# Kernel tuning notes

Measured on AMD Instinct MI355X. Metric: run time of the kernel, lower is better.

## Reference

```python
import jax, jax.numpy as jnp
import numpy as np

D_MODEL = 1024
NUM_HEADS = 16
D_K = D_MODEL // NUM_HEADS
ROPE_THETA = 10000.0


def setup_inputs() -> dict:
    key = jax.random.key(0)
    kx, kq, kk, kv, ko = jax.random.split(key, 5)
    B, S = 4, 2048
    std = (2.0 / (D_MODEL + D_MODEL)) ** 0.5
    def w(k):
        return jax.random.truncated_normal(k, -3.0, 3.0, (D_MODEL, D_MODEL), jnp.float32) * std
    return {
        "x": jax.random.normal(kx, (B, S, D_MODEL), jnp.float32),
        "Wq": w(kq), "Wk": w(kk), "Wv": w(kv), "Wo": w(ko),
    }


def _apply_rope(t):
    # t: [B, H, S, d_k]
    S, dk = t.shape[-2], t.shape[-1]
    inv_freq = 1.0 / (ROPE_THETA ** (jnp.arange(0, dk, 2) / dk))  # [dk/2]
    angles = jnp.outer(jnp.arange(S), inv_freq)                    # [S, dk/2]
    cos = jnp.repeat(jnp.cos(angles), 2, axis=-1).astype(t.dtype)  # [S, dk]
    sin = jnp.repeat(jnp.sin(angles), 2, axis=-1).astype(t.dtype)
    t_even = t[..., 0::2]
    t_odd = t[..., 1::2]
    t_rot = jnp.stack([-t_odd, t_even], axis=-1).reshape(t.shape)
    return t * cos + t_rot * sin


def reference(x, Wq, Wk, Wv, Wo):
    B, S, D = x.shape
    H, dk = NUM_HEADS, D_K
    q = jnp.einsum("bsi,io->bso", x, Wq).reshape(B, S, H, dk).swapaxes(1, 2)
    k = jnp.einsum("bsi,io->bso", x, Wk).reshape(B, S, H, dk).swapaxes(1, 2)
    v = jnp.einsum("bsi,io->bso", x, Wv).reshape(B, S, H, dk).swapaxes(1, 2)
    q = _apply_rope(q)
    k = _apply_rope(k)
    scores = jnp.einsum("bhqd,bhkd->bhqk", q, k) / (dk ** 0.5)  # [B,H,S,S]
    causal = jnp.tril(jnp.ones((S, S), dtype=bool))
    scores = jnp.where(causal, scores, -jnp.inf)
    attn = jax.nn.softmax(scores, axis=-1)
    out = jnp.einsum("bhqk,bhkd->bhqd", attn, v)  # [B,H,S,dk]
    out = out.swapaxes(1, 2).reshape(B, S, D)
    return jnp.einsum("bsi,io->bso", out, Wo)
```

## Files before the change

### kernel.cpp

```cpp
#include <hip/hip_runtime.h>
#include <hip/hip_bf16.h>

#define SEQ   2048
#define NB    4
#define NH    16
#define DK    64
#define DM    1024
#define MROWS (NB * SEQ)
#define WEL   (DM * DM)

typedef __bf16 bf16_t;
typedef __bf16 bf16x8 __attribute__((ext_vector_type(8)));
typedef __bf16 bf16x4 __attribute__((ext_vector_type(4)));
typedef float  f32x4  __attribute__((ext_vector_type(4)));

#define MFMA16(a, b, c) __builtin_amdgcn_mfma_f32_16x16x32_bf16((a), (b), (c), 0, 0, 0)

__device__ __forceinline__ void gl2lds16(const bf16_t* g, bf16_t* l) {
    __builtin_amdgcn_global_load_lds(
        (const __attribute__((address_space(1))) unsigned int*)g,
        (__attribute__((address_space(3))) unsigned int*)l, 16, 0, 0);
}

#define BAR()   __builtin_amdgcn_s_barrier()
#define SCB()   __builtin_amdgcn_sched_barrier(0)
#define LGK0()  asm volatile("s_waitcnt lgkmcnt(0)")
#define LGK8()  asm volatile("s_waitcnt lgkmcnt(8)")
#define VMC(N)  asm volatile("s_waitcnt vmcnt(" #N ")")

__global__ __launch_bounds__(256) void prep_kernel(
    const float* __restrict__ x,
    const float* __restrict__ Wq, const float* __restrict__ Wk,
    const float* __restrict__ Wv, const float* __restrict__ Wo,
    bf16_t* __restrict__ xb, bf16_t* __restrict__ Wqkvt,
    bf16_t* __restrict__ Wot, float2* __restrict__ rope)
{
    __shared__ float T[32][33];
    const int bid = blockIdx.x;
    const int tid = threadIdx.x;

    if (bid < 8192) {
        const int i = (bid * 256 + tid) * 4;
        const float4 v = *(const float4*)(x + i);
        bf16x4 o;
        o[0] = (bf16_t)v.x; o[1] = (bf16_t)v.y;
        o[2] = (bf16_t)v.z; o[3] = (bf16_t)v.w;
        *(bf16x4*)(xb + i) = o;
    } else if (bid < 12288) {
        const int wb = bid - 8192;
        const int w  = wb >> 10;
        const int b10 = wb & 1023;
        const float* W = (w == 0) ? Wq : (w == 1) ? Wk : (w == 2) ? Wv : Wo;
        bf16_t* Wt = (w == 3) ? Wot : Wqkvt + (size_t)w * WEL;
        const int tk0 = (b10 >> 5) << 5;
        const int tn0 = (b10 & 31) << 5;
        const int r = tid >> 5, c = tid & 31;
#pragma unroll
        for (int i = 0; i < 4; ++i)
            T[r + i * 8][c] = W[(size_t)(tk0 + r + i * 8) * DM + tn0 + c];
        __syncthreads();
#pragma unroll
        for (int i = 0; i < 4; ++i)
            Wt[(size_t)(tn0 + r + i * 8) * DM + tk0 + c] = (bf16_t)T[c][r + i * 8];
    } else {
        const int idx = (bid - 12288) * 256 + tid;
        const int s = idx >> 5, i = idx & 31;
        const float freq = powf(10000.0f, -(float)i / 32.0f);
        const float a = (float)s * freq;
        rope[idx] = make_float2(cosf(a), sinf(a));
    }
}

template<bool TR>
__device__ __forceinline__ void kloop(
    const bf16_t* __restrict__ Xp, const bf16_t* __restrict__ Wp,
    bf16_t* L, int tid, f32x4 (&acc)[8][4])
{
    const int lane = tid & 63;
    const int wave = tid >> 6;
    const int wm   = wave >> 2;
    const int wn   = wave & 3;
    const int lrow = lane & 15;
    const int lcol = (lane >> 4) << 3;

    bf16_t* const AR = L;
    bf16_t* const BR = L + 32768;

    const bf16_t* pA0 = Xp + (size_t)(wave * 16 + lrow) * DM + lcol;
    const bf16_t* pA1 = pA0 + (size_t)128 * DM;
    const bf16_t* pB0 = Wp + (size_t)(wave * 16 + lrow) * DM + lcol;
    const bf16_t* pB1 = pB0 + (size_t)128 * DM;

    bf16_t* const adst = AR + wave * 1024;
    bf16_t* const bdst = BR + wave * 1024;

    const bf16_t* const Ard = AR + wm * 8192;
    const bf16_t* const Brd = BR + wn * 4096;

    bf16x8 a[2][2], bc[4][2];

#define RD_A(BUF, Q)                                                          \
    a[0][0] = *(const bf16x8*)(Ard + (BUF) + (2*(Q)+0)*1024 + lane*8);        \
    a[0][1] = *(const bf16x8*)(Ard + (BUF) + (2*(Q)+0)*1024 + 512 + lane*8);  \
    a[1][0] = *(const bf16x8*)(Ard + (BUF) + (2*(Q)+1)*1024 + lane*8);        \
    a[1][1] = *(const bf16x8*)(Ard + (BUF) + (2*(Q)+1)*1024 + 512 + lane*8);

#define RD_B(BUF, NF)                                                         \
    bc[NF][0] = *(const bf16x8*)(Brd + (BUF) + (NF)*1024 + lane*8);           \
    bc[NF][1] = *(const bf16x8*)(Brd + (BUF) + (NF)*1024 + 512 + lane*8);

#define ST_A(BUF, H, C)                                                       \
    gl2lds16(((H) ? pA1 : pA0) + (C),      adst + (BUF) + (H)*8192);          \
    gl2lds16(((H) ? pA1 : pA0) + (C) + 32, adst + (BUF) + (H)*8192 + 512);

#define ST_B(BUF, H, C)                                                       \
    gl2lds16(((H) ? pB1 : pB0) + (C),      bdst + (BUF) + (H)*8192);          \
    gl2lds16(((H) ? pB1 : pB0) + (C) + 32, bdst + (BUF) + (H)*8192 + 512);

#define QMMA(Q)                                                               \
    __builtin_amdgcn_s_setprio(1);                                            \
    _Pragma("unroll")                                                         \
    for (int nf = 0; nf < 4; ++nf) {                                          \
        if (TR) {                                                             \
            acc[2*(Q)][nf]   = MFMA16(bc[nf][0], a[0][0], acc[2*(Q)][nf]);    \
            acc[2*(Q)][nf]   = MFMA16(bc[nf][1], a[0][1], acc[2*(Q)][nf]);    \
            acc[2*(Q)+1][nf] = MFMA16(bc[nf][0], a[1][0], acc[2*(Q)+1][nf]);  \
            acc[2*(Q)+1][nf] = MFMA16(bc[nf][1], a[1][1], acc[2*(Q)+1][nf]);  \
        } else {                                                              \
            acc[2*(Q)][nf]   = MFMA16(a[0][0], bc[nf][0], acc[2*(Q)][nf]);    \
            acc[2*(Q)][nf]   = MFMA16(a[0][1], bc[nf][1], acc[2*(Q)][nf]);    \
            acc[2*(Q)+1][nf] = MFMA16(a[1][0], bc[nf][0], acc[2*(Q)+1][nf]);  \
            acc[2*(Q)+1][nf] = MFMA16(a[1][1], bc[nf][1], acc[2*(Q)+1][nf]);  \
        }                                                                     \
    }                                                                         \
    __builtin_amdgcn_s_setprio(0);

    ST_B(0, 0, 0)      ST_B(0, 1, 0)
    ST_A(0, 0, 0)      ST_A(0, 1, 0)
    ST_B(16384, 0, 64) ST_B(16384, 1, 64)
    VMC(4);
    BAR();

    for (int it = 0; it < 8; ++it) {
        const bool lst = (it == 7);

        RD_A(0, 0) RD_B(0, 0) RD_B(0, 1) RD_B(0, 2) RD_B(0, 3)
        ST_A(16384, 0, 64) ST_A(16384, 1, 64)
        LGK8();
        BAR(); LGK0(); SCB();
        QMMA(0)
        BAR();

        RD_A(0, 1)
        if (!lst) { ST_B(0, 0, 128) }
        BAR(); LGK0(); SCB();
        QMMA(1)
        BAR();

        RD_A(0, 2)
        if (!lst) { ST_B(0, 1, 128) }
        BAR(); LGK0(); SCB();
        QMMA(2)
        BAR();

        RD_A(0, 3)
        BAR(); LGK0(); SCB();
        QMMA(3)
        if (lst) { VMC(0); } else { VMC(4); }
        BAR();

        RD_A(16384, 0) RD_B(16384, 0) RD_B(16384, 1) RD_B(16384, 2) RD_B(16384, 3)
        if (!lst) { ST_A(0, 0, 128) }
        LGK8();
        BAR(); LGK0(); SCB();
        QMMA(0)
        BAR();

        RD_A(16384, 1)
        if (!lst) { ST_A(0, 1, 128) }
        BAR(); LGK0(); SCB();
        QMMA(1)
        BAR();

        RD_A(16384, 2)
        if (!lst) { ST_B(16384, 0, 192) }
        BAR(); LGK0(); SCB();
        QMMA(2)
        BAR();

        RD_A(16384, 3)
        if (!lst) { ST_B(16384, 1, 192) }
        BAR(); LGK0(); SCB();
        QMMA(3)
        if (!lst) { VMC(4); }
        BAR();

        pA0 += 128; pA1 += 128; pB0 += 128; pB1 += 128;
    }

#undef QMMA
#undef ST_B
#undef ST_A
#undef RD_B
#undef RD_A
}

__global__ __launch_bounds__(512, 2) void gemm_qkv_kernel(
    const bf16_t* __restrict__ X, const bf16_t* __restrict__ Wt,
    bf16_t* __restrict__ Qt, bf16_t* __restrict__ Kt, bf16_t* __restrict__ Vtr,
    const float2* __restrict__ rope)
{
    __shared__ __align__(16) bf16_t L[65536];

    const int tid = threadIdx.x;
    const int xcd = blockIdx.x & 7;
    const int idx = blockIdx.x >> 3;
    const int mt  = xcd * 4 + (idx & 3);
    const int nt  = idx >> 2;
    const int m0 = mt << 8, n0 = nt << 8;
    const bool tr = (n0 >= 2 * DM);

    f32x4 acc[8][4] = {};
    if (tr) kloop<true >(X + (size_t)m0 * DM, Wt + (size_t)n0 * DM, L, tid, acc);
    else    kloop<false>(X + (size_t)m0 * DM, Wt + (size_t)n0 * DM, L, tid, acc);

    const int lane = tid & 63;
    const int wave = tid >> 6;
    const int wm   = wave >> 2, wn = wave & 3;
    const int l    = lane & 15;
    const int quad = lane >> 4;

#pragma unroll
    for (int mf = 0; mf < 8; ++mf)
#pragma unroll
        for (int nf = 0; nf < 4; ++nf)
#pragma unroll
            for (int r = 0; r < 4; ++r) {
                float v = acc[mf][nf][r];
                if (tr) {
                    const int n = n0 + wn * 64 + nf * 16 + quad * 4 + r;
                    const int m = m0 + wm * 128 + mf * 16 + l;
                    const int bi = m >> 11, s = m & (SEQ - 1);
                    const int col = n & (DM - 1);
                    const int h = col >> 6, d = col & (DK - 1);
                    Vtr[(((size_t)(bi * NH + h)) * DK + d) * SEQ + s] = (bf16_t)v;
                } else {
                    const int m  = m0 + wm * 128 + mf * 16 + quad * 4 + r;
                    const int nn = n0 + wn * 64 + nf * 16 + l;
                    const int bi = m >> 11, s = m & (SEQ - 1);
                    const int col = nn & (DM - 1);
                    const int h = col >> 6, d = col & (DK - 1);
                    float pv = __shfl_xor(v, 1);
                    float2 cs = rope[s * 32 + (d >> 1)];
                    float res = (d & 1) ? (v * cs.x + pv * cs.y)
                                        : (v * cs.x - pv * cs.y);
                    bf16_t* dst = (nn < DM) ? Qt : Kt;
                    if (nn < DM) res *= 0.125f;
                    dst[(((size_t)(bi * NH + h)) * SEQ + s) * DK + d] = (bf16_t)res;
                }
            }
}

__global__ __launch_bounds__(512, 2) void gemm_out_kernel(
    const bf16_t* __restrict__ X, const bf16_t* __restrict__ Wt,
    float* __restrict__ out)
{
    __shared__ __align__(16) bf16_t L[49152];

    const int tid = threadIdx.x;
    const int xcd = blockIdx.x & 7;
    const int idx = blockIdx.x >> 3;
    const int mt  = xcd * 8 + (idx & 7);
    const int nt  = idx >> 3;
    const int m0 = mt << 7, n0 = nt << 8;

    const int lane = tid & 63;
    const int wave = tid >> 6;
    const int wm   = wave >> 2;
    const int wn   = wave & 3;
    const int lrow = lane & 15;
    const int lcol = (lane >> 4) << 3;

    bf16_t* const AR = L;
    bf16_t* const BR = L + 16384;

    const bf16_t* Xp = X + (size_t)m0 * DM;
    const bf16_t* Wp = Wt + (size_t)n0 * DM;
    const bf16_t* pA  = Xp + (size_t)(wave * 16 + lrow) * DM + lcol;
    const bf16_t* pB0 = Wp + (size_t)(wave * 16 + lrow) * DM + lcol;
    const bf16_t* pB1 = pB0 + (size_t)128 * DM;

    bf16_t* const adst = AR + wave * 1024;
    bf16_t* const bdst = BR + wave * 1024;

    const bf16_t* const Ard = AR + wm * 4096;
    const bf16_t* const Brd = BR + wn * 4096;

    f32x4 acc[4][4] = {};
    bf16x8 a[2][2], bc[4][2];

#define RD_AH(BUF, Q)                                                         \
    a[0][0] = *(const bf16x8*)(Ard + (BUF) + (2*(Q)+0)*1024 + lane*8);        \
    a[0][1] = *(const bf16x8*)(Ard + (BUF) + (2*(Q)+0)*1024 + 512 + lane*8);  \
    a[1][0] = *(const bf16x8*)(Ard + (BUF) + (2*(Q)+1)*1024 + lane*8);        \
    a[1][1] = *(const bf16x8*)(Ard + (BUF) + (2*(Q)+1)*1024 + 512 + lane*8);

#define RD_BH(BUF, NF)                                                        \
    bc[NF][0] = *(const bf16x8*)(Brd + (BUF) + (NF)*1024 + lane*8);           \
    bc[NF][1] = *(const bf16x8*)(Brd + (BUF) + (NF)*1024 + 512 + lane*8);

#define ST_AH(BUF, C)                                                         \
    gl2lds16(pA + (C),      adst + (BUF));                                    \
    gl2lds16(pA + (C) + 32, adst + (BUF) + 512);

#define ST_BH(BUF, H, C)                                                      \
    gl2lds16(((H) ? pB1 : pB0) + (C),      bdst + (BUF) + (H)*8192);          \
    gl2lds16(((H) ? pB1 : pB0) + (C) + 32, bdst + (BUF) + (H)*8192 + 512);

#define QMMAH(Q)                                                              \
    __builtin_amdgcn_s_setprio(1);                                            \
    _Pragma("unroll")                                                         \
    for (int nf = 0; nf < 4; ++nf) {                                          \
        acc[2*(Q)][nf]   = MFMA16(a[0][0], bc[nf][0], acc[2*(Q)][nf]);        \
        acc[2*(Q)][nf]   = MFMA16(a[0][1], bc[nf][1], acc[2*(Q)][nf]);        \
        acc[2*(Q)+1][nf] = MFMA16(a[1][0], bc[nf][0], acc[2*(Q)+1][nf]);      \
        acc[2*(Q)+1][nf] = MFMA16(a[1][1], bc[nf][1], acc[2*(Q)+1][nf]);      \
    }                                                                         \
    __builtin_amdgcn_s_setprio(0);

    ST_AH(0, 0)
    ST_BH(0, 0, 0) ST_BH(0, 1, 0)
    ST_BH(16384, 0, 64) ST_BH(16384, 1, 64)
    VMC(4);
    BAR();

    for (int it = 0; it < 8; ++it) {
        const bool lst = (it == 7);

        RD_AH(0, 0) RD_BH(0, 0) RD_BH(0, 1) RD_BH(0, 2) RD_BH(0, 3)
        ST_AH(8192, 64)
        LGK8();
        BAR(); LGK0(); SCB();
        QMMAH(0)
        BAR();
        RD_AH(0, 1)
        if (!lst) { ST_BH(0, 0, 128) ST_BH(0, 1, 128) }
        BAR(); LGK0(); SCB();
        QMMAH(1)
        if (lst) { VMC(0); } else { VMC(4); }
        BAR();

        RD_AH(8192, 0) RD_BH(16384, 0) RD_BH(16384, 1) RD_BH(16384, 2) RD_BH(16384, 3)
        if (!lst) { ST_AH(0, 128) }
        LGK8();
        BAR(); LGK0(); SCB();
        QMMAH(0)
        BAR();
        RD_AH(8192, 1)
        if (!lst) { ST_BH(16384, 0, 192) ST_BH(16384, 1, 192) }
        BAR(); LGK0(); SCB();
        QMMAH(1)
        if (!lst) { VMC(4); }
        BAR();

        pA += 128; pB0 += 128; pB1 += 128;
    }

#undef QMMAH
#undef ST_BH
#undef ST_AH
#undef RD_BH
#undef RD_AH

    const int l    = lane & 15;
    const int quad = lane >> 4;
#pragma unroll
    for (int mf = 0; mf < 4; ++mf)
#pragma unroll
        for (int nf = 0; nf < 4; ++nf)
#pragma unroll
            for (int r = 0; r < 4; ++r) {
                const int m  = m0 + wm * 64 + mf * 16 + quad * 4 + r;
                const int nn = n0 + wn * 64 + nf * 16 + l;
                out[(size_t)m * DM + nn] = acc[mf][nf][r];
            }
}

#define KLD  72
#define KVSZ (64 * KLD)

__global__ __launch_bounds__(256) void attn_kernel(
    const bf16_t* __restrict__ Q, const bf16_t* __restrict__ K,
    const bf16_t* __restrict__ Vt, bf16_t* __restrict__ O)
{
    __shared__ __align__(16) bf16_t Kl[2 * KVSZ];
    __shared__ __align__(16) bf16_t Vl[2 * KVSZ];
    __shared__ __align__(16) bf16_t Pl[4][32 * KLD];

    const int bh   = blockIdx.x;
    const int qx   = blockIdx.y;
    const int tid  = threadIdx.x;
    const int wave = tid >> 6;
    const int lane = tid & 63;
    const int l    = lane & 15;
    const int quad = lane >> 4;
    const int srow = tid >> 3;
    const int sch  = (tid & 7) << 3;

    bf16_t* Pw = Pl[wave];
    const bf16_t* Qb = Q  + (size_t)bh * SEQ * DK;
    const bf16_t* Kb = K  + (size_t)bh * SEQ * DK;
    const bf16_t* Vb = Vt + (size_t)bh * DK * SEQ;
    const int b = bh >> 4, h = bh & 15;

    for (int ph = 0; ph < 2; ++ph) {
        const int qblk = ph ? (15 - qx) : qx;
        const int q0w  = qblk * 128 + wave * 32;
        const int nch  = 2 * (qblk + 1);

        bf16x8 qb[2][2];
#pragma unroll
        for (int u = 0; u < 2; ++u) {
            qb[u][0] = *(const bf16x8*)(Qb + (size_t)(q0w + u * 16 + l) * DK + quad * 8);
            qb[u][1] = *(const bf16x8*)(Qb + (size_t)(q0w + u * 16 + l) * DK + 32 + quad * 8);
        }

        float m_run[2] = {-3e38f, -3e38f};
        float l_run[2] = {0.f, 0.f};
        f32x4 o[4][2] = {};

        bf16x8 pk0 = *(const bf16x8*)(Kb + (size_t)srow * DK + sch);
        bf16x8 pk1 = *(const bf16x8*)(Kb + (size_t)(32 + srow) * DK + sch);
        bf16x8 pv0 = *(const bf16x8*)(Vb + (size_t)srow * SEQ + sch);
        bf16x8 pv1 = *(const bf16x8*)(Vb + (size_t)(32 + srow) * SEQ + sch);
        __syncthreads();
        *(bf16x8*)(Kl + srow * KLD + sch)        = pk0;
        *(bf16x8*)(Kl + (32 + srow) * KLD + sch) = pk1;
        *(bf16x8*)(Vl + srow * KLD + sch)        = pv0;
        *(bf16x8*)(Vl + (32 + srow) * KLD + sch) = pv1;
        __syncthreads();

        for (int i = 0; i < nch; ++i) {
            const int c  = i * 64;
            const int bf = (i & 1) * KVSZ;
            const int bn = ((i & 1) ^ 1) * KVSZ;
            const bool pf = (i + 1 < nch);

            if (pf) {
                const int cn = c + 64;
                pk0 = *(const bf16x8*)(Kb + (size_t)(cn + srow) * DK + sch);
                pk1 = *(const bf16x8*)(Kb + (size_t)(cn + 32 + srow) * DK + sch);
                pv0 = *(const bf16x8*)(Vb + (size_t)srow * SEQ + cn + sch);
                pv1 = *(const bf16x8*)(Vb + (size_t)(32 + srow) * SEQ + cn + sch);
            }

            if (c <= q0w + 31) {
                const bf16_t* Klb = Kl + bf;
                const bf16_t* Vlb = Vl + bf;

                f32x4 st[4][2] = {};
                __builtin_amdgcn_s_setprio(1);
#pragma unroll
                for (int t = 0; t < 4; ++t) {
                    const bf16x8 k0 = *(const bf16x8*)(Klb + (t * 16 + l) * KLD + quad * 8);
                    const bf16x8 k1 = *(const bf16x8*)(Klb + (t * 16 + l) * KLD + 32 + quad * 8);
                    st[t][0] = MFMA16(k0, qb[0][0], st[t][0]);
                    st[t][0] = MFMA16(k1, qb[0][1], st[t][0]);
                    st[t][1] = MFMA16(k0, qb[1][0], st[t][1]);
                    st[t][1] = MFMA16(k1, qb[1][1], st[t][1]);
                }
                __builtin_amdgcn_s_setprio(0);
                if (c + 63 > q0w) {
#pragma unroll
                    for (int u = 0; u < 2; ++u) {
                        const int thr = q0w + u * 16 + l - c - quad * 4;
#pragma unroll
                        for (int t = 0; t < 4; ++t)
#pragma unroll
                            for (int r = 0; r < 4; ++r)
                                if (t * 16 + r > thr) st[t][u][r] = -3e38f;
                    }
                }
#pragma unroll
                for (int u = 0; u < 2; ++u) {
                    float cmax = -3e38f;
#pragma unroll
                    for (int t = 0; t < 4; ++t)
#pragma unroll
                        for (int r = 0; r < 4; ++r)
                            cmax = fmaxf(cmax, st[t][u][r]);
                    cmax = fmaxf(cmax, __shfl_xor(cmax, 16));
                    cmax = fmaxf(cmax, __shfl_xor(cmax, 32));
                    if (!__all(cmax - m_run[u] <= 8.0f)) {
                        const float mnew  = fmaxf(m_run[u], cmax);
                        const float alpha = __expf(m_run[u] - mnew);
                        m_run[u] = mnew;
                        l_run[u] *= alpha;
#pragma unroll
                        for (int n = 0; n < 4; ++n)
#pragma unroll
                            for (int r = 0; r < 4; ++r)
                                o[n][u][r] *= alpha;
                    }
                    float csum = 0.f;
#pragma unroll
                    for (int t = 0; t < 4; ++t)
#pragma unroll
                        for (int r = 0; r < 4; ++r) {
                            st[t][u][r] = __expf(st[t][u][r] - m_run[u]);
                            csum += st[t][u][r];
                        }
                    csum += __shfl_xor(csum, 16);
                    csum += __shfl_xor(csum, 32);
                    l_run[u] += csum;
#pragma unroll
                    for (int t = 0; t < 4; ++t) {
                        bf16x4 pk;
                        pk[0] = (bf16_t)st[t][u][0]; pk[1] = (bf16_t)st[t][u][1];
                        pk[2] = (bf16_t)st[t][u][2]; pk[3] = (bf16_t)st[t][u][3];
                        *(bf16x4*)(Pw + (u * 16 + l) * KLD + t * 16 + quad * 4) = pk;
                    }
                }
                const bf16x8 pb00 = *(const bf16x8*)(Pw + l * KLD + quad * 8);
                const bf16x8 pb01 = *(const bf16x8*)(Pw + l * KLD + 32 + quad * 8);
                const bf16x8 pb10 = *(const bf16x8*)(Pw + (16 + l) * KLD + quad * 8);
                const bf16x8 pb11 = *(const bf16x8*)(Pw + (16 + l) * KLD + 32 + quad * 8);
                __builtin_amdgcn_s_setprio(1);
#pragma unroll
                for (int n = 0; n < 4; ++n) {
                    const bf16x8 v0 = *(const bf16x8*)(Vlb + (n * 16 + l) * KLD + quad * 8);
                    const bf16x8 v1 = *(const bf16x8*)(Vlb + (n * 16 + l) * KLD + 32 + quad * 8);
                    o[n][0] = MFMA16(v0, pb00, o[n][0]);
                    o[n][0] = MFMA16(v1, pb01, o[n][0]);
                    o[n][1] = MFMA16(v0, pb10, o[n][1]);
                    o[n][1] = MFMA16(v1, pb11, o[n][1]);
                }
                __builtin_amdgcn_s_setprio(0);
            }

            if (pf) {
                *(bf16x8*)(Kl + bn + srow * KLD + sch)        = pk0;
                *(bf16x8*)(Kl + bn + (32 + srow) * KLD + sch) = pk1;
                *(bf16x8*)(Vl + bn + srow * KLD + sch)        = pv0;
                *(bf16x8*)(Vl + bn + (32 + srow) * KLD + sch) = pv1;
            }
            __syncthreads();
        }

#pragma unroll
        for (int u = 0; u < 2; ++u) {
            const float inv = 1.0f / l_run[u];
#pragma unroll
            for (int n = 0; n < 4; ++n) {
                bf16x4 ov;
                ov[0] = (bf16_t)(o[n][u][0] * inv); ov[1] = (bf16_t)(o[n][u][1] * inv);
                ov[2] = (bf16_t)(o[n][u][2] * inv); ov[3] = (bf16_t)(o[n][u][3] * inv);
                *(bf16x4*)(Pw + (u * 16 + l) * KLD + n * 16 + quad * 4) = ov;
            }
        }
        const int row  = lane >> 1;
        const int half = (lane & 1) * 32;
        const bf16x8 w0 = *(const bf16x8*)(Pw + row * KLD + half);
        const bf16x8 w1 = *(const bf16x8*)(Pw + row * KLD + half + 8);
        const bf16x8 w2 = *(const bf16x8*)(Pw + row * KLD + half + 16);
        const bf16x8 w3 = *(const bf16x8*)(Pw + row * KLD + half + 24);
        bf16_t* op = O + ((size_t)(b * SEQ + qblk * 128 + wave * 32 + row)) * DM
                       + h * DK + half;
        *(bf16x8*)(op)      = w0;
        *(bf16x8*)(op + 8)  = w1;
        *(bf16x8*)(op + 16) = w2;
        *(bf16x8*)(op + 24) = w3;
    }
}

extern "C" void kernel_launch(void* const* d_in, const int* in_sizes, int n_in,
                              void* d_out, int out_size, void* d_ws, size_t ws_size,
                              hipStream_t stream)
{
    const float* x  = (const float*)d_in[0];
    const float* Wq = (const float*)d_in[1];
    const float* Wk = (const float*)d_in[2];
    const float* Wv = (const float*)d_in[3];
    const float* Wo = (const float*)d_in[4];

    char* ws = (char*)d_ws;
    float2* rope = (float2*)ws;
    const size_t TEN = (size_t)MROWS * DM;
    bf16_t* xb    = (bf16_t*)(ws + (1 << 19));
    bf16_t* Wqkvt = xb + TEN;
    bf16_t* Wot   = Wqkvt + 3 * (size_t)WEL;
    bf16_t* Qt    = Wot + WEL;
    bf16_t* Kt    = Qt + TEN;
    bf16_t* Vt    = Kt + TEN;
    bf16_t* Ot    = Vt + TEN;

    prep_kernel<<<12544, 256, 0, stream>>>(x, Wq, Wk, Wv, Wo,
                                           xb, Wqkvt, Wot, rope);

    gemm_qkv_kernel<<<32 * 12, 512, 0, stream>>>(xb, Wqkvt, Qt, Kt, Vt, rope);

    attn_kernel<<<dim3(NB * NH, 8), 256, 0, stream>>>(Qt, Kt, Vt, Ot);

    gemm_out_kernel<<<64 * 4, 512, 0, stream>>>(Ot, Wot, (float*)d_out);
}
```

Baseline: 294.3 us.

## Merge GEMM MFMA phases to halve barriers and change attention LDS padding

The QKV GEMM main loop now loads two A fragments into separate register sets (a0/a1) and issues two QMMA quarter-steps per barrier phase. This halves the number of barrier/LDS-wait phases per K-step, and global-to-LDS stores are grouped in pairs to match. The redundant lgkmcnt(8) waits are dropped from both GEMM kernels, and setprio now wraps the larger MFMA groups. Separately, the attention kernel's LDS row stride drops from 72 to 66 bf16 to change bank mapping and LDS footprint. That stride leaves 16-byte vector LDS reads misaligned, and the doubled A registers add register pressure.

New measurement: 449.5 us. +52.7%, slower.

```diff
diff --git a/kernel.cpp b/kernel.cpp
--- a/kernel.cpp
+++ b/kernel.cpp
@@ -25,7 +25,6 @@
 #define BAR()   __builtin_amdgcn_s_barrier()
 #define SCB()   __builtin_amdgcn_sched_barrier(0)
 #define LGK0()  asm volatile("s_waitcnt lgkmcnt(0)")
-#define LGK8()  asm volatile("s_waitcnt lgkmcnt(8)")
 #define VMC(N)  asm volatile("s_waitcnt vmcnt(" #N ")")
 
 __global__ __launch_bounds__(256) void prep_kernel(
@@ -97,13 +96,13 @@
     const bf16_t* const Ard = AR + wm * 8192;
     const bf16_t* const Brd = BR + wn * 4096;
 
-    bf16x8 a[2][2], bc[4][2];
-
-#define RD_A(BUF, Q)                                                          \
-    a[0][0] = *(const bf16x8*)(Ard + (BUF) + (2*(Q)+0)*1024 + lane*8);        \
-    a[0][1] = *(const bf16x8*)(Ard + (BUF) + (2*(Q)+0)*1024 + 512 + lane*8);  \
-    a[1][0] = *(const bf16x8*)(Ard + (BUF) + (2*(Q)+1)*1024 + lane*8);        \
-    a[1][1] = *(const bf16x8*)(Ard + (BUF) + (2*(Q)+1)*1024 + 512 + lane*8);
+    bf16x8 a0[2][2], a1[2][2], bc[4][2];
+
+#define RD_A(BUF, Q, D)                                                       \
+    D[0][0] = *(const bf16x8*)(Ard + (BUF) + (2*(Q)+0)*1024 + lane*8);        \
+    D[0][1] = *(const bf16x8*)(Ard + (BUF) + (2*(Q)+0)*1024 + 512 + lane*8);  \
+    D[1][0] = *(const bf16x8*)(Ard + (BUF) + (2*(Q)+1)*1024 + lane*8);        \
+    D[1][1] = *(const bf16x8*)(Ard + (BUF) + (2*(Q)+1)*1024 + 512 + lane*8);
 
 #define RD_B(BUF, NF)                                                         \
     bc[NF][0] = *(const bf16x8*)(Brd + (BUF) + (NF)*1024 + lane*8);           \
@@ -117,23 +116,21 @@
     gl2lds16(((H) ? pB1 : pB0) + (C),      bdst + (BUF) + (H)*8192);          \
     gl2lds16(((H) ? pB1 : pB0) + (C) + 32, bdst + (BUF) + (H)*8192 + 512);
 
-#define QMMA(Q)                                                               \
-    __builtin_amdgcn_s_setprio(1);                                            \
+#define QMMA(Q, A)                                                            \
     _Pragma("unroll")                                                         \
     for (int nf = 0; nf < 4; ++nf) {                                          \
         if (TR) {                                                             \
-            acc[2*(Q)][nf]   = MFMA16(bc[nf][0], a[0][0], acc[2*(Q)][nf]);    \
-            acc[2*(Q)][nf]   = MFMA16(bc[nf][1], a[0][1], acc[2*(Q)][nf]);    \
-            acc[2*(Q)+1][nf] = MFMA16(bc[nf][0], a[1][0], acc[2*(Q)+1][nf]);  \
-            acc[2*(Q)+1][nf] = MFMA16(bc[nf][1], a[1][1], acc[2*(Q)+1][nf]);  \
+            acc[2*(Q)][nf]   = MFMA16(bc[nf][0], A[0][0], acc[2*(Q)][nf]);    \
+            acc[2*(Q)][nf]   = MFMA16(bc[nf][1], A[0][1], acc[2*(Q)][nf]);    \
+            acc[2*(Q)+1][nf] = MFMA16(bc[nf][0], A[1][0], acc[2*(Q)+1][nf]);  \
+            acc[2*(Q)+1][nf] = MFMA16(bc[nf][1], A[1][1], acc[2*(Q)+1][nf]);  \
         } else {                                                              \
-            acc[2*(Q)][nf]   = MFMA16(a[0][0], bc[nf][0], acc[2*(Q)][nf]);    \
-            acc[2*(Q)][nf]   = MFMA16(a[0][1], bc[nf][1], acc[2*(Q)][nf]);    \
-            acc[2*(Q)+1][nf] = MFMA16(a[1][0], bc[nf][0], acc[2*(Q)+1][nf]);  \
-            acc[2*(Q)+1][nf] = MFMA16(a[1][1], bc[nf][1], acc[2*(Q)+1][nf]);  \
+            acc[2*(Q)][nf]   = MFMA16(A[0][0], bc[nf][0], acc[2*(Q)][nf]);    \
+            acc[2*(Q)][nf]   = MFMA16(A[0][1], bc[nf][1], acc[2*(Q)][nf]);    \
+            acc[2*(Q)+1][nf] = MFMA16(A[1][0], bc[nf][0], acc[2*(Q)+1][nf]);  \
+            acc[2*(Q)+1][nf] = MFMA16(A[1][1], bc[nf][1], acc[2*(Q)+1][nf]);  \
         }                                                                     \
-    }                                                                         \
-    __builtin_amdgcn_s_setprio(0);
+    }
 
     ST_B(0, 0, 0)      ST_B(0, 1, 0)
     ST_A(0, 0, 0)      ST_A(0, 1, 0)
@@ -144,54 +141,39 @@
     for (int it = 0; it < 8; ++it) {
         const bool lst = (it == 7);
 
-        RD_A(0, 0) RD_B(0, 0) RD_B(0, 1) RD_B(0, 2) RD_B(0, 3)
+        RD_A(0, 0, a0) RD_A(0, 1, a1)
+        RD_B(0, 0) RD_B(0, 1) RD_B(0, 2) RD_B(0, 3)
         ST_A(16384, 0, 64) ST_A(16384, 1, 64)
-        LGK8();
-        BAR(); LGK0(); SCB();
-        QMMA(0)
-        BAR();
-
-        RD_A(0, 1)
-        if (!lst) { ST_B(0, 0, 128) }
-        BAR(); LGK0(); SCB();
-        QMMA(1)
-        BAR();
-
-        RD_A(0, 2)
-        if (!lst) { ST_B(0, 1, 128) }
-        BAR(); LGK0(); SCB();
-        QMMA(2)
-        BAR();
-
-        RD_A(0, 3)
-        BAR(); LGK0(); SCB();
-        QMMA(3)
+        BAR(); LGK0(); SCB();
+        __builtin_amdgcn_s_setprio(1);
+        QMMA(0, a0) QMMA(1, a1)
+        __builtin_amdgcn_s_setprio(0);
+        BAR();
+
+        RD_A(0, 2, a0) RD_A(0, 3, a1)
+        if (!lst) { ST_B(0, 0, 128) ST_B(0, 1, 128) }
+        BAR(); LGK0(); SCB();
+        __builtin_amdgcn_s_setprio(1);
+        QMMA(2, a0) QMMA(3, a1)
+        __builtin_amdgcn_s_setprio(0);
         if (lst) { VMC(0); } else { VMC(4); }
         BAR();
 
-        RD_A(16384, 0) RD_B(16384, 0) RD_B(16384, 1) RD_B(16384, 2) RD_B(16384, 3)
-        if (!lst) { ST_A(0, 0, 128) }
-        LGK8();
-        BAR(); LGK0(); SCB();
-        QMMA(0)
-        BAR();
-
-        RD_A(16384, 1)
-        if (!lst) { ST_A(0, 1, 128) }
-        BAR(); LGK0(); SCB();
-        QMMA(1)
-        BAR();
-
-        RD_A(16384, 2)
-        if (!lst) { ST_B(16384, 0, 192) }
-        BAR(); LGK0(); SCB();
-        QMMA(2)
-        BAR();
-
-        RD_A(16384, 3)
-        if (!lst) { ST_B(16384, 1, 192) }
-        BAR(); LGK0(); SCB();
-        QMMA(3)
+        RD_A(16384, 0, a0) RD_A(16384, 1, a1)
+        RD_B(16384, 0) RD_B(16384, 1) RD_B(16384, 2) RD_B(16384, 3)
+        if (!lst) { ST_A(0, 0, 128) ST_A(0, 1, 128) }
+        BAR(); LGK0(); SCB();
+        __builtin_amdgcn_s_setprio(1);
+        QMMA(0, a0) QMMA(1, a1)
+        __builtin_amdgcn_s_setprio(0);
+        BAR();
+
+        RD_A(16384, 2, a0) RD_A(16384, 3, a1)
+        if (!lst) { ST_B(16384, 0, 192) ST_B(16384, 1, 192) }
+        BAR(); LGK0(); SCB();
+        __builtin_amdgcn_s_setprio(1);
+        QMMA(2, a0) QMMA(3, a1)
+        __builtin_amdgcn_s_setprio(0);
         if (!lst) { VMC(4); }
         BAR();
 
@@ -339,7 +321,6 @@
 
         RD_AH(0, 0) RD_BH(0, 0) RD_BH(0, 1) RD_BH(0, 2) RD_BH(0, 3)
         ST_AH(8192, 64)
-        LGK8();
         BAR(); LGK0(); SCB();
         QMMAH(0)
         BAR();
@@ -352,7 +333,6 @@
 
         RD_AH(8192, 0) RD_BH(16384, 0) RD_BH(16384, 1) RD_BH(16384, 2) RD_BH(16384, 3)
         if (!lst) { ST_AH(0, 128) }
-        LGK8();
         BAR(); LGK0(); SCB();
         QMMAH(0)
         BAR();
@@ -386,7 +366,7 @@
             }
 }
 
-#define KLD  72
+#define KLD  66
 #define KVSZ (64 * KLD)
 
 __global__ __launch_bounds__(256) void attn_kernel(
```
